# Kernel tuning notes

Hardware: AMD Instinct MI355X
Metric: run time of the kernel (lower is better)

The kernel has to match this reference:

```python
import jax, jax.numpy as jnp
import numpy as np

D = 2048
NUM_HEADS = 16
HEAD_DIM = D // NUM_HEADS
B, T = 4, 2048
NEG = -1e9


def setup_inputs() -> dict:
    key = jax.random.key(0)
    ks = jax.random.split(key, 6)
    X = jax.random.normal(ks[0], (B, T, D), dtype=jnp.float32)
    # additive causal mask, broadcast over batch and heads
    causal = jnp.tril(jnp.ones((T, T), dtype=jnp.float32))
    mask = jnp.where(causal == 1, 0.0, NEG)[None, None, :, :]
    scale = np.sqrt(2.0 / D).astype(np.float32)
    wq_w = jax.random.normal(ks[1], (D, D), dtype=jnp.float32) * scale
    wk_w = jax.random.normal(ks[2], (D, D), dtype=jnp.float32) * scale
    wv_w = jax.random.normal(ks[3], (D, D), dtype=jnp.float32) * scale
    wo_w = jax.random.normal(ks[4], (D, D), dtype=jnp.float32) * scale
    zeros = jnp.zeros((D,), dtype=jnp.float32)
    return {
        "X": X, "mask": mask,
        "wq_w": wq_w, "wq_b": zeros,
        "wk_w": wk_w, "wk_b": zeros,
        "wv_w": wv_w, "wv_b": zeros,
        "wo_w": wo_w, "wo_b": zeros,
    }


def reference(X, mask, wq_w, wq_b, wk_w, wk_b, wv_w, wv_b, wo_w, wo_b):
    b, t, d = X.shape
    # project and split heads: [b, h, t, hd]
    def proj(w, bias):
        return (X @ w + bias).reshape(b, t, NUM_HEADS, HEAD_DIM).transpose(0, 2, 1, 3)
    Q = proj(wq_w, wq_b)
    K = proj(wk_w, wk_b)
    V = proj(wv_w, wv_b)
    scores = jnp.einsum("bhqd,bhkd->bhqk", Q, K) / np.sqrt(HEAD_DIM).astype(X.dtype)
    scores = scores + mask
    A = jax.nn.softmax(scores, axis=-1)
    ctx = jnp.einsum("bhqk,bhkd->bhqd", A, V)  # [b, h, t, hd]
    ctx = ctx.transpose(0, 2, 1, 3).reshape(b, t, d)
    return ctx @ wo_w + wo_b
```

## Files before the change

### kernel.cpp

```cpp
#include <hip/hip_runtime.h>
#include <stdint.h>

#define DMODEL 2048
#define NH 16
#define HD 128
#define BATCH 4
#define SEQ 2048
#define MTOT (BATCH * SEQ)
#define LOG2E 1.44269504088896340736f

typedef __bf16 bf16x8 __attribute__((ext_vector_type(8)));
typedef float floatx4 __attribute__((ext_vector_type(4)));

__device__ __forceinline__ uint16_t f2b(float f) {
    union { float f; uint32_t i; } v; v.f = f;
    uint32_t r = v.i + 0x7fffu + ((v.i >> 16) & 1u);
    return (uint16_t)(r >> 16);
}

#define GLD16(gp, lp)                                                          \
    __builtin_amdgcn_global_load_lds(                                          \
        (__attribute__((address_space(1))) unsigned int*)(gp),                 \
        (__attribute__((address_space(3))) unsigned int*)(lp), 16, 0, 0)

__global__ __launch_bounds__(256) void cvt_bf16(const float* __restrict__ in,
                                                uint16_t* __restrict__ out, int n) {
    const int i = (blockIdx.x * 256 + threadIdx.x) * 8;
    if (i >= n) return;
    const float4 a = *(const float4*)(in + i);
    const float4 b = *(const float4*)(in + i + 4);
    uint16_t v[8] __attribute__((aligned(16))) = {
        f2b(a.x), f2b(a.y), f2b(a.z), f2b(a.w),
        f2b(b.x), f2b(b.y), f2b(b.z), f2b(b.w)};
    *(uint4*)(out + i) = *(const uint4*)v;
}

__global__ __launch_bounds__(256) void tr_wf(const float* __restrict__ in,
                                             uint16_t* __restrict__ out) {
    __shared__ float t[64 * 69];
    const int tid = threadIdx.x;
    const int r0 = blockIdx.y * 64, c0 = blockIdx.x * 64;
    const int rr = tid >> 2, c16 = (tid & 3) << 4;
#pragma unroll
    for (int j = 0; j < 4; j++)
        *(float4*)&t[rr * 69 + c16 + j * 4] =
            *(const float4*)(in + (size_t)(r0 + rr) * DMODEL + c0 + c16 + j * 4);
    __syncthreads();
    const int oc = tid >> 2, r16 = (tid & 3) << 4;
    uint16_t v[16] __attribute__((aligned(16)));
#pragma unroll
    for (int j = 0; j < 16; j++) v[j] = f2b(t[(r16 + j) * 69 + oc]);
    uint16_t* o = out + (size_t)(c0 + oc) * DMODEL + r0 + r16;
    *(uint4*)o = *(const uint4*)v;
    *(uint4*)(o + 8) = *(const uint4*)(v + 8);
}

__global__ __launch_bounds__(256, 2) void gemm(const uint16_t* __restrict__ A,
                                               const uint16_t* __restrict__ Bt,
                                               const float* __restrict__ bias,
                                               void* __restrict__ Cout,
                                               float scale, int out_f32) {
    __shared__ __attribute__((aligned(16))) uint16_t As[128 * 32];
    __shared__ __attribute__((aligned(16))) uint16_t Bs[128 * 32];
    const int tid = threadIdx.x, lane = tid & 63, w = tid >> 6;
    const int wr = w >> 1, wc = w & 1;
    const int col = lane & 15, quad = lane >> 4;
    const long m0 = (long)blockIdx.y * 128, n0 = (long)blockIdx.x * 128;

    floatx4 acc[4][4];
#pragma unroll
    for (int i = 0; i < 4; i++)
#pragma unroll
        for (int j = 0; j < 4; j++) acc[i][j] = (floatx4){0.f, 0.f, 0.f, 0.f};

    const int srow = tid >> 2, sc = (tid & 3) << 3;
    const uint16_t* Ag0 = A + (m0 + srow) * DMODEL + sc;
    const uint16_t* Bg0 = Bt + (n0 + srow) * DMODEL + sc;
    const long rstep = (long)64 * DMODEL;
    uint16_t* AsW = &As[w * 512];
    uint16_t* BsW = &Bs[w * 512];

    for (int kt = 0; kt < DMODEL; kt += 32) {
        GLD16(Ag0 + kt, AsW);
        GLD16(Ag0 + rstep + kt, AsW + 2048);
        GLD16(Bg0 + kt, BsW);
        GLD16(Bg0 + rstep + kt, BsW + 2048);
        __syncthreads();
        bf16x8 af[4], bfr[4];
#pragma unroll
        for (int i = 0; i < 4; i++)
            af[i] = *(const bf16x8*)&As[(wr * 64 + i * 16 + col) * 32 + quad * 8];
#pragma unroll
        for (int j = 0; j < 4; j++)
            bfr[j] = *(const bf16x8*)&Bs[(wc * 64 + j * 16 + col) * 32 + quad * 8];
#pragma unroll
        for (int i = 0; i < 4; i++)
#pragma unroll
            for (int j = 0; j < 4; j++)
                acc[i][j] = __builtin_amdgcn_mfma_f32_16x16x32_bf16(af[i], bfr[j],
                                                                    acc[i][j], 0, 0, 0);
        __syncthreads();
    }

    float bv[4];
#pragma unroll
    for (int j = 0; j < 4; j++) bv[j] = bias[n0 + wc * 64 + j * 16 + col];
#pragma unroll
    for (int i = 0; i < 4; i++) {
        const long row = m0 + wr * 64 + i * 16 + quad * 4;
#pragma unroll
        for (int j = 0; j < 4; j++) {
            const long cc = n0 + wc * 64 + j * 16 + col;
#pragma unroll
            for (int r = 0; r < 4; r++) {
                const float v = (acc[i][j][r] + bv[j]) * scale;
                const long idx = (row + r) * DMODEL + cc;
                if (out_f32) ((float*)Cout)[idx] = v;
                else         ((uint16_t*)Cout)[idx] = f2b(v);
            }
        }
    }
}

__global__ __launch_bounds__(256, 2) void flash(uint16_t* __restrict__ QO,
                                                const uint16_t* __restrict__ Kp,
                                                const uint16_t* __restrict__ Vp) {
    __shared__ __attribute__((aligned(16))) uint16_t Ks[4 * 64 * 32];
    __shared__ __attribute__((aligned(16))) uint16_t Vs[2 * 128 * 32];
    __shared__ __attribute__((aligned(16))) uint16_t Ps[4][32 * 88];

    const int tid = threadIdx.x, lane = tid & 63, w = tid >> 6;
    const int col = lane & 15, quad = lane >> 4;
    const int h = blockIdx.y & 15, b = blockIdx.y >> 4;
    const size_t brow = (size_t)b * SEQ;

    const uint16_t* kbase = Kp + brow * DMODEL + h * HD;
    const uint16_t* vbase = Vp + brow * DMODEL + h * HD;
    const int srow = tid >> 2;
    const int sc8 = (tid & 3) << 3;

    for (int half = 0; half < 2; ++half) {
        const int qi = half ? (int)blockIdx.x : (15 - (int)blockIdx.x);
        const int q0 = qi * 128;
        uint16_t* qbase = QO + (brow + q0 + w * 32) * DMODEL + h * HD;

        bf16x8 qf[2][4];
#pragma unroll
        for (int i = 0; i < 2; i++)
#pragma unroll
            for (int kk = 0; kk < 4; kk++)
                qf[i][kk] = *(const bf16x8*)(qbase + (size_t)(i * 16 + col) * DMODEL +
                                             kk * 32 + quad * 8);

        floatx4 accO[2][8];
#pragma unroll
        for (int i = 0; i < 2; i++)
#pragma unroll
            for (int jd = 0; jd < 8; jd++) accO[i][jd] = (floatx4){0.f, 0.f, 0.f, 0.f};
        float mrun[2][4], lrun[2][4];
#pragma unroll
        for (int i = 0; i < 2; i++)
#pragma unroll
            for (int r = 0; r < 4; r++) { mrun[i][r] = -1e30f; lrun[i][r] = 0.f; }

        const int nkt = 2 * qi + 2;

        uint4 kv[4], vv4[4];
        {
            const uint16_t* kg = kbase + (size_t)srow * DMODEL + sc8;
            const uint16_t* vg = vbase + (size_t)srow * DMODEL + sc8;
#pragma unroll
            for (int p = 0; p < 4; p++) {
                kv[p] = *(const uint4*)(kg + p * 32);
                vv4[p] = *(const uint4*)(vg + p * 32);
            }
        }

        for (int ki = 0; ki < nkt; ki++) {
            const int key0 = ki * 64;
#pragma unroll
            for (int p = 0; p < 4; p++)
                *(uint4*)&Ks[(p * 256 + tid) * 8] = kv[p];
            {
                const int vb0 = ((srow >> 5) * 128) * 32 + (srow & 31);
#pragma unroll
                for (int p = 0; p < 4; p++) {
                    uint16_t vals[8] __attribute__((aligned(16)));
                    *(uint4*)vals = vv4[p];
                    const int d0 = sc8 + p * 32;
#pragma unroll
                    for (int j = 0; j < 8; j++) Vs[vb0 + (d0 + j) * 32] = vals[j];
                }
            }
            __syncthreads();

            if (ki + 1 < nkt) {
                const uint16_t* kg = kbase + (size_t)(key0 + 64 + srow) * DMODEL + sc8;
                const uint16_t* vg = vbase + (size_t)(key0 + 64 + srow) * DMODEL + sc8;
#pragma unroll
                for (int p = 0; p < 4; p++) {
                    kv[p] = *(const uint4*)(kg + p * 32);
                    vv4[p] = *(const uint4*)(vg + p * 32);
                }
            }

            floatx4 s[2][4];
#pragma unroll
            for (int i = 0; i < 2; i++)
#pragma unroll
                for (int jk = 0; jk < 4; jk++) {
                    floatx4 a = (floatx4){0.f, 0.f, 0.f, 0.f};
#pragma unroll
                    for (int kk = 0; kk < 4; kk++) {
                        bf16x8 bb = *(const bf16x8*)&Ks[(kk * 64 + jk * 16 + col) * 32 + quad * 8];
                        a = __builtin_amdgcn_mfma_f32_16x16x32_bf16(qf[i][kk], bb, a, 0, 0, 0);
                    }
                    s[i][jk] = a;
                }

            if (key0 + 63 > q0 + w * 32) {
#pragma unroll
                for (int i = 0; i < 2; i++) {
                    const int qb = q0 + w * 32 + i * 16 + quad * 4;
#pragma unroll
                    for (int jk = 0; jk < 4; jk++) {
                        const int key = key0 + jk * 16 + col;
#pragma unroll
                        for (int r = 0; r < 4; r++)
                            if (key > qb + r) s[i][jk][r] = -1e30f;
                    }
                }
            }

            float alpha[2][4];
#pragma unroll
            for (int i = 0; i < 2; i++)
#pragma unroll
                for (int r = 0; r < 4; r++) {
                    float mx = s[i][0][r];
#pragma unroll
                    for (int jk = 1; jk < 4; jk++) mx = fmaxf(mx, s[i][jk][r]);
                    mx = fmaxf(mx, __shfl_xor(mx, 1, 64));
                    mx = fmaxf(mx, __shfl_xor(mx, 2, 64));
                    mx = fmaxf(mx, __shfl_xor(mx, 4, 64));
                    mx = fmaxf(mx, __shfl_xor(mx, 8, 64));
                    mx = fmaxf(mx, mrun[i][r]);
                    alpha[i][r] = exp2f((mrun[i][r] - mx) * LOG2E);
                    mrun[i][r] = mx;
                }
#pragma unroll
            for (int i = 0; i < 2; i++)
#pragma unroll
                for (int r = 0; r < 4; r++) {
                    float psum = 0.f;
#pragma unroll
                    for (int jk = 0; jk < 4; jk++) {
                        const float p = exp2f((s[i][jk][r] - mrun[i][r]) * LOG2E);
                        psum += p;
                        Ps[w][(i * 16 + quad * 4 + r) * 88 + jk * 16 + col] = f2b(p);
                    }
                    lrun[i][r] = lrun[i][r] * alpha[i][r] + psum;
                }
#pragma unroll
            for (int i = 0; i < 2; i++)
#pragma unroll
                for (int jd = 0; jd < 8; jd++)
#pragma unroll
                    for (int r = 0; r < 4; r++) accO[i][jd][r] *= alpha[i][r];

            bf16x8 pf[2][2];
#pragma unroll
            for (int i = 0; i < 2; i++)
#pragma unroll
                for (int k2 = 0; k2 < 2; k2++)
                    pf[i][k2] = *(const bf16x8*)&Ps[w][(i * 16 + col) * 88 + k2 * 32 + quad * 8];
#pragma unroll
            for (int i = 0; i < 2; i++)
#pragma unroll
                for (int jd = 0; jd < 8; jd++)
#pragma unroll
                    for (int k2 = 0; k2 < 2; k2++) {
                        bf16x8 vvv = *(const bf16x8*)&Vs[(k2 * 128 + jd * 16 + col) * 32 + quad * 8];
                        accO[i][jd] = __builtin_amdgcn_mfma_f32_16x16x32_bf16(pf[i][k2], vvv,
                                                                              accO[i][jd], 0, 0, 0);
                    }
            __syncthreads();
        }

        float inv[2][4];
#pragma unroll
        for (int i = 0; i < 2; i++)
#pragma unroll
            for (int r = 0; r < 4; r++) {
                float l = lrun[i][r];
                l += __shfl_xor(l, 1, 64);
                l += __shfl_xor(l, 2, 64);
                l += __shfl_xor(l, 4, 64);
                l += __shfl_xor(l, 8, 64);
                inv[i][r] = 1.0f / l;
            }
#pragma unroll
        for (int i = 0; i < 2; i++)
#pragma unroll
            for (int jd = 0; jd < 8; jd++)
#pragma unroll
                for (int r = 0; r < 4; r++)
                    qbase[(size_t)(i * 16 + quad * 4 + r) * DMODEL + jd * 16 + col] =
                        f2b(accO[i][jd][r] * inv[i][r]);
    }
}

extern "C" void kernel_launch(void* const* d_in, const int* in_sizes, int n_in,
                              void* d_out, int out_size, void* d_ws, size_t ws_size,
                              hipStream_t stream) {
    const float* X   = (const float*)d_in[0];
    float*       msk = (float*)d_in[1];
    const float* wq  = (const float*)d_in[2];
    const float* wqb = (const float*)d_in[3];
    const float* wk  = (const float*)d_in[4];
    const float* wkb = (const float*)d_in[5];
    const float* wv  = (const float*)d_in[6];
    const float* wvb = (const float*)d_in[7];
    const float* wo  = (const float*)d_in[8];
    const float* wob = (const float*)d_in[9];
    float* out = (float*)d_out;

    char* ws = (char*)d_ws;
    const size_t MB = 1ull << 20;
    dim3 tb(256), gT(32, 32);
    const float qs = 0.08838834764831845f;

    if (ws_size >= 136 * MB) {
        uint16_t* Xb = (uint16_t*)(ws);
        uint16_t* Qb = (uint16_t*)(ws + 32 * MB);
        uint16_t* Kb = (uint16_t*)(ws + 64 * MB);
        uint16_t* Vb = (uint16_t*)(ws + 96 * MB);
        uint16_t* Wt = (uint16_t*)(ws + 128 * MB);
        dim3 gG(16, 64), gF(8, 64);
        cvt_bf16<<<8192, tb, 0, stream>>>(X, Xb, MTOT * DMODEL);
        tr_wf<<<gT, tb, 0, stream>>>(wq, Wt);
        gemm<<<gG, tb, 0, stream>>>(Xb, Wt, wqb, Qb, qs, 0);
        tr_wf<<<gT, tb, 0, stream>>>(wk, Wt);
        gemm<<<gG, tb, 0, stream>>>(Xb, Wt, wkb, Kb, 1.0f, 0);
        tr_wf<<<gT, tb, 0, stream>>>(wv, Wt);
        gemm<<<gG, tb, 0, stream>>>(Xb, Wt, wvb, Vb, 1.0f, 0);
        flash<<<gF, tb, 0, stream>>>(Qb, Kb, Vb);
        tr_wf<<<gT, tb, 0, stream>>>(wo, Wt);
        gemm<<<gG, tb, 0, stream>>>(Qb, Wt, wob, out, 1.0f, 1);
    } else {
        uint16_t* Xb = (uint16_t*)(ws);
        uint16_t* Qb = (uint16_t*)(ws + 8 * MB);
        uint16_t *Kb, *Vb, *Wt;
        if (ws_size >= 40 * MB) {
            Kb = (uint16_t*)(ws + 16 * MB);
            Vb = (uint16_t*)(ws + 24 * MB);
            Wt = (uint16_t*)(ws + 32 * MB);
        } else {
            Kb = (uint16_t*)msk;
            Vb = Kb + (size_t)SEQ * DMODEL;
            Wt = (uint16_t*)(ws + 16 * MB);
        }
        dim3 gG(16, 16), gF(8, 16);
        for (int b = 0; b < BATCH; b++) {
            const float* Xf = X + (size_t)b * SEQ * DMODEL;
            float* Ob = out + (size_t)b * SEQ * DMODEL;
            cvt_bf16<<<2048, tb, 0, stream>>>(Xf, Xb, SEQ * DMODEL);
            tr_wf<<<gT, tb, 0, stream>>>(wq, Wt);
            gemm<<<gG, tb, 0, stream>>>(Xb, Wt, wqb, Qb, qs, 0);
            tr_wf<<<gT, tb, 0, stream>>>(wk, Wt);
            gemm<<<gG, tb, 0, stream>>>(Xb, Wt, wkb, Kb, 1.0f, 0);
            tr_wf<<<gT, tb, 0, stream>>>(wv, Wt);
            gemm<<<gG, tb, 0, stream>>>(Xb, Wt, wvb, Vb, 1.0f, 0);
            flash<<<gF, tb, 0, stream>>>(Qb, Kb, Vb);
            tr_wf<<<gT, tb, 0, stream>>>(wo, Wt);
            gemm<<<gG, tb, 0, stream>>>(Qb, Wt, wob, Ob, 1.0f, 1);
        }
    }

    (void)in_sizes; (void)n_in; (void)out_size;
}
```

Baseline: 760.4 us.

## Write V transposed from projection GEMM so flash loads V rows directly

The V projection GEMM gains a mode that writes its output transposed (head-dim major, token minor). The flash kernel can then fill its V shared-memory tile with 16-byte vector stores instead of eight scalar 2-byte scattered stores per thread. The PV MFMA loop is reordered so each V fragment read from LDS serves both row blocks, and MFMA sections are wrapped in s_setprio to favour the matrix work. The transposed epilogue writes only 8-byte chunks with a large stride, which may make the V GEMM's stores less coalesced.

```diff
diff --git a/kernel.cpp b/kernel.cpp
--- a/kernel.cpp
+++ b/kernel.cpp
@@ -59,7 +59,7 @@
                                                const uint16_t* __restrict__ Bt,
                                                const float* __restrict__ bias,
                                                void* __restrict__ Cout,
-                                               float scale, int out_f32) {
+                                               float scale, int mode, int tld) {
     __shared__ __attribute__((aligned(16))) uint16_t As[128 * 32];
     __shared__ __attribute__((aligned(16))) uint16_t Bs[128 * 32];
     const int tid = threadIdx.x, lane = tid & 63, w = tid >> 6;
@@ -111,12 +111,21 @@
 #pragma unroll
         for (int j = 0; j < 4; j++) {
             const long cc = n0 + wc * 64 + j * 16 + col;
-#pragma unroll
-            for (int r = 0; r < 4; r++) {
-                const float v = (acc[i][j][r] + bv[j]) * scale;
-                const long idx = (row + r) * DMODEL + cc;
-                if (out_f32) ((float*)Cout)[idx] = v;
-                else         ((uint16_t*)Cout)[idx] = f2b(v);
+            if (mode == 2) {
+                uint16_t tmp[4] __attribute__((aligned(8)));
+#pragma unroll
+                for (int r = 0; r < 4; r++)
+                    tmp[r] = f2b((acc[i][j][r] + bv[j]) * scale);
+                *(uint2*)&((uint16_t*)Cout)[(size_t)cc * tld + row] =
+                    *(const uint2*)tmp;
+            } else {
+#pragma unroll
+                for (int r = 0; r < 4; r++) {
+                    const float v = (acc[i][j][r] + bv[j]) * scale;
+                    const long idx = (row + r) * DMODEL + cc;
+                    if (mode == 1) ((float*)Cout)[idx] = v;
+                    else           ((uint16_t*)Cout)[idx] = f2b(v);
+                }
             }
         }
     }
@@ -124,7 +133,8 @@
 
 __global__ __launch_bounds__(256, 2) void flash(uint16_t* __restrict__ QO,
                                                 const uint16_t* __restrict__ Kp,
-                                                const uint16_t* __restrict__ Vp) {
+                                                const uint16_t* __restrict__ Vt,
+                                                int vld) {
     __shared__ __attribute__((aligned(16))) uint16_t Ks[4 * 64 * 32];
     __shared__ __attribute__((aligned(16))) uint16_t Vs[2 * 128 * 32];
     __shared__ __attribute__((aligned(16))) uint16_t Ps[4][32 * 88];
@@ -135,9 +145,11 @@
     const size_t brow = (size_t)b * SEQ;
 
     const uint16_t* kbase = Kp + brow * DMODEL + h * HD;
-    const uint16_t* vbase = Vp + brow * DMODEL + h * HD;
+    const uint16_t* vtbase = Vt + (size_t)(h * HD) * vld + brow;
     const int srow = tid >> 2;
     const int sc8 = (tid & 3) << 3;
+    const int vd = tid >> 3;
+    const int vkc = tid & 7;
 
     for (int half = 0; half < 2; ++half) {
         const int qi = half ? (int)blockIdx.x : (15 - (int)blockIdx.x);
@@ -168,12 +180,12 @@
         uint4 kv[4], vv4[4];
         {
             const uint16_t* kg = kbase + (size_t)srow * DMODEL + sc8;
-            const uint16_t* vg = vbase + (size_t)srow * DMODEL + sc8;
-#pragma unroll
-            for (int p = 0; p < 4; p++) {
-                kv[p] = *(const uint4*)(kg + p * 32);
-                vv4[p] = *(const uint4*)(vg + p * 32);
-            }
+#pragma unroll
+            for (int p = 0; p < 4; p++) kv[p] = *(const uint4*)(kg + p * 32);
+#pragma unroll
+            for (int it = 0; it < 4; it++)
+                vv4[it] = *(const uint4*)(vtbase + (size_t)(it * 32 + vd) * vld +
+                                          vkc * 8);
         }
 
         for (int ki = 0; ki < nkt; ki++) {
@@ -181,30 +193,24 @@
 #pragma unroll
             for (int p = 0; p < 4; p++)
                 *(uint4*)&Ks[(p * 256 + tid) * 8] = kv[p];
-            {
-                const int vb0 = ((srow >> 5) * 128) * 32 + (srow & 31);
-#pragma unroll
-                for (int p = 0; p < 4; p++) {
-                    uint16_t vals[8] __attribute__((aligned(16)));
-                    *(uint4*)vals = vv4[p];
-                    const int d0 = sc8 + p * 32;
-#pragma unroll
-                    for (int j = 0; j < 8; j++) Vs[vb0 + (d0 + j) * 32] = vals[j];
-                }
-            }
+#pragma unroll
+            for (int it = 0; it < 4; it++)
+                *(uint4*)&Vs[((vkc >> 2) * 128 + it * 32 + vd) * 32 + (vkc & 3) * 8] =
+                    vv4[it];
             __syncthreads();
 
             if (ki + 1 < nkt) {
                 const uint16_t* kg = kbase + (size_t)(key0 + 64 + srow) * DMODEL + sc8;
-                const uint16_t* vg = vbase + (size_t)(key0 + 64 + srow) * DMODEL + sc8;
-#pragma unroll
-                for (int p = 0; p < 4; p++) {
-                    kv[p] = *(const uint4*)(kg + p * 32);
-                    vv4[p] = *(const uint4*)(vg + p * 32);
-                }
+#pragma unroll
+                for (int p = 0; p < 4; p++) kv[p] = *(const uint4*)(kg + p * 32);
+#pragma unroll
+                for (int it = 0; it < 4; it++)
+                    vv4[it] = *(const uint4*)(vtbase + (size_t)(it * 32 + vd) * vld +
+                                              key0 + 64 + vkc * 8);
             }
 
             floatx4 s[2][4];
+            __builtin_amdgcn_s_setprio(1);
 #pragma unroll
             for (int i = 0; i < 2; i++)
 #pragma unroll
@@ -217,6 +223,7 @@
                     }
                     s[i][jk] = a;
                 }
+            __builtin_amdgcn_s_setprio(0);
 
             if (key0 + 63 > q0 + w * 32) {
 #pragma unroll
@@ -274,16 +281,18 @@
 #pragma unroll
                 for (int k2 = 0; k2 < 2; k2++)
                     pf[i][k2] = *(const bf16x8*)&Ps[w][(i * 16 + col) * 88 + k2 * 32 + quad * 8];
-#pragma unroll
-            for (int i = 0; i < 2; i++)
-#pragma unroll
-                for (int jd = 0; jd < 8; jd++)
-#pragma unroll
-                    for (int k2 = 0; k2 < 2; k2++) {
-                        bf16x8 vvv = *(const bf16x8*)&Vs[(k2 * 128 + jd * 16 + col) * 32 + quad * 8];
+            __builtin_amdgcn_s_setprio(1);
+#pragma unroll
+            for (int jd = 0; jd < 8; jd++)
+#pragma unroll
+                for (int k2 = 0; k2 < 2; k2++) {
+                    bf16x8 vvv = *(const bf16x8*)&Vs[(k2 * 128 + jd * 16 + col) * 32 + quad * 8];
+#pragma unroll
+                    for (int i = 0; i < 2; i++)
                         accO[i][jd] = __builtin_amdgcn_mfma_f32_16x16x32_bf16(pf[i][k2], vvv,
                                                                               accO[i][jd], 0, 0, 0);
-                    }
+                }
+            __builtin_amdgcn_s_setprio(0);
             __syncthreads();
         }
 
@@ -339,14 +348,14 @@
         dim3 gG(16, 64), gF(8, 64);
         cvt_bf16<<<8192, tb, 0, stream>>>(X, Xb, MTOT * DMODEL);
         tr_wf<<<gT, tb, 0, stream>>>(wq, Wt);
-        gemm<<<gG, tb, 0, stream>>>(Xb, Wt, wqb, Qb, qs, 0);
+        gemm<<<gG, tb, 0, stream>>>(Xb, Wt, wqb, Qb, qs, 0, 0);
         tr_wf<<<gT, tb, 0, stream>>>(wk, Wt);
-        gemm<<<gG, tb, 0, stream>>>(Xb, Wt, wkb, Kb, 1.0f, 0);
+        gemm<<<gG, tb, 0, stream>>>(Xb, Wt, wkb, Kb, 1.0f, 0, 0);
         tr_wf<<<gT, tb, 0, stream>>>(wv, Wt);
-        gemm<<<gG, tb, 0, stream>>>(Xb, Wt, wvb, Vb, 1.0f, 0);
-        flash<<<gF, tb, 0, stream>>>(Qb, Kb, Vb);
+        gemm<<<gG, tb, 0, stream>>>(Xb, Wt, wvb, Vb, 1.0f, 2, MTOT);
+        flash<<<gF, tb, 0, stream>>>(Qb, Kb, Vb, MTOT);
         tr_wf<<<gT, tb, 0, stream>>>(wo, Wt);
-        gemm<<<gG, tb, 0, stream>>>(Qb, Wt, wob, out, 1.0f, 1);
+        gemm<<<gG, tb, 0, stream>>>(Qb, Wt, wob, out, 1.0f, 1, 0);
     } else {
         uint16_t* Xb = (uint16_t*)(ws);
         uint16_t* Qb = (uint16_t*)(ws + 8 * MB);
@@ -366,14 +375,14 @@
             float* Ob = out + (size_t)b * SEQ * DMODEL;
             cvt_bf16<<<2048, tb, 0, stream>>>(Xf, Xb, SEQ * DMODEL);
             tr_wf<<<gT, tb, 0, stream>>>(wq, Wt);
-            gemm<<<gG, tb, 0, stream>>>(Xb, Wt, wqb, Qb, qs, 0);
+            gemm<<<gG, tb, 0, stream>>>(Xb, Wt, wqb, Qb, qs, 0, 0);
             tr_wf<<<gT, tb, 0, stream>>>(wk, Wt);
-            gemm<<<gG, tb, 0, stream>>>(Xb, Wt, wkb, Kb, 1.0f, 0);
+            gemm<<<gG, tb, 0, stream>>>(Xb, Wt, wkb, Kb, 1.0f, 0, 0);
             tr_wf<<<gT, tb, 0, stream>>>(wv, Wt);
-            gemm<<<gG, tb, 0, stream>>>(Xb, Wt, wvb, Vb, 1.0f, 0);
-            flash<<<gF, tb, 0, stream>>>(Qb, Kb, Vb);
+            gemm<<<gG, tb, 0, stream>>>(Xb, Wt, wvb, Vb, 1.0f, 2, SEQ);
+            flash<<<gF, tb, 0, stream>>>(Qb, Kb, Vb, SEQ);
             tr_wf<<<gT, tb, 0, stream>>>(wo, Wt);
-            gemm<<<gG, tb, 0, stream>>>(Qb, Wt, wob, Ob, 1.0f, 1);
+            gemm<<<gG, tb, 0, stream>>>(Qb, Wt, wob, Ob, 1.0f, 1, 0);
         }
     }
 
```

Result: no change. 750.5 us (-1.3%).
